# Optimization experiments

Hardware: AMD Instinct MI355X
Metric: run time of the kernel (lower is better)

## Reference

```python
import jax, jax.numpy as jnp
import numpy as np

H = 8
D = 512  # dmodel; each naive head projects to full D (not D//H)


def setup_inputs() -> dict:
    key = jax.random.key(0)
    ks = jax.random.split(key, 9)
    s = 1.0 / np.sqrt(D)
    x = jax.random.normal(ks[0], (2, 2048, D), dtype=jnp.float32)
    Wq = jax.random.normal(ks[1], (H, D, D), dtype=jnp.float32) * s
    Wk = jax.random.normal(ks[2], (H, D, D), dtype=jnp.float32) * s
    Wv = jax.random.normal(ks[3], (H, D, D), dtype=jnp.float32) * s
    bq = jnp.zeros((H, D), dtype=jnp.float32)
    bk = jnp.zeros((H, D), dtype=jnp.float32)
    bv = jnp.zeros((H, D), dtype=jnp.float32)
    Wo = jax.random.normal(ks[4], (H * D, D), dtype=jnp.float32) * (1.0 / np.sqrt(H * D))
    bo = jnp.zeros((D,), dtype=jnp.float32)
    return {"x": x, "Wq": Wq, "Wk": Wk, "Wv": Wv, "bq": bq, "bk": bk, "bv": bv, "Wo": Wo, "bo": bo}


def reference(x, Wq, Wk, Wv, bq, bk, bv, Wo, bo):
    # Batched form of the per-head Python loop: q/k/v -> [b, h, s, d]
    q = jnp.einsum("bsd,hde->bhse", x, Wq) + bq[None, :, None, :]
    k = jnp.einsum("bsd,hde->bhse", x, Wk) + bk[None, :, None, :]
    v = jnp.einsum("bsd,hde->bhse", x, Wv) + bv[None, :, None, :]
    scale = 1.0 / jnp.sqrt(jnp.asarray(D, dtype=x.dtype))
    scores = jnp.einsum("bhqe,bhke->bhqk", q, k) * scale  # [b, h, s, s]
    attn = jax.nn.softmax(scores, axis=-1)
    heads = jnp.einsum("bhqk,bhke->bhqe", attn, v)  # [b, h, s, d]
    b, h, s, d = heads.shape
    concat = jnp.transpose(heads, (0, 2, 1, 3)).reshape(b, s, h * d)  # concat on last axis
    out = concat @ Wo + bo  # output projection
    return out + x  # residual add
```

## Files before the change

### kernel.cpp

```cpp
#include <hip/hip_runtime.h>

typedef unsigned short u16;
typedef __attribute__((ext_vector_type(8))) short bh8;
typedef __attribute__((ext_vector_type(4))) float f32x4;
typedef __attribute__((ext_vector_type(4))) u16 us4;
typedef __attribute__((ext_vector_type(8))) u16 us8;

__device__ __forceinline__ u16 f2bf(float f){
  unsigned u = __builtin_bit_cast(unsigned, f);
  u += 0x7fffu + ((u >> 16) & 1u);
  return (u16)(u >> 16);
}
__device__ __forceinline__ float bf2f(u16 b){
  unsigned u = ((unsigned)b) << 16;
  return __builtin_bit_cast(float, u);
}

__device__ __forceinline__ void gload16(const void* g, void* l){
  __builtin_amdgcn_global_load_lds((const __attribute__((address_space(1))) unsigned*)g,
                                   (__attribute__((address_space(3))) unsigned*)l, 16, 0, 0);
}

template<int OUT_MODE>
__device__ __forceinline__ void gemm_core(
    u16* As, u16* Bs,
    const u16* __restrict__ A, int lda,
    const u16* __restrict__ B, int ldb,
    int K, float scale,
    const float* __restrict__ bias,
    float* __restrict__ lsum,
    const float* __restrict__ lraw,
    u16* __restrict__ outB, int ldo,
    int m0, int n0)
{
  const int t  = threadIdx.x;
  const int ln = t & 63;
  const int wv = t >> 6;
  const int wr = wv >> 1;
  const int wc = wv & 1;

  const int rs = t >> 2;
  const int cs = (t & 3) * 8;
  const u16* Ag0 = A + (size_t)(m0 + rs) * lda + cs;
  const u16* Ag1 = Ag0 + (size_t)64 * lda;
  const u16* Bg0 = B + (size_t)(n0 + rs) * ldb + cs;
  const u16* Bg1 = Bg0 + (size_t)64 * ldb;
  char* lA0 = (char*)As + wv * 1024;
  char* lA1 = lA0 + 4096;
  char* lB0 = (char*)Bs + wv * 1024;
  char* lB1 = lB0 + 4096;

  f32x4 acc[4][4] = {};

  const int frow = (ln & 15);
  const int fk   = (ln >> 4) * 8;

  for (int k0 = 0; k0 < K; k0 += 32){
    gload16(Ag0 + k0, lA0);
    gload16(Ag1 + k0, lA1);
    gload16(Bg0 + k0, lB0);
    gload16(Bg1 + k0, lB1);
    __syncthreads();
    bh8 a[4], b[4];
#pragma unroll
    for (int i = 0; i < 4; i++)
      a[i] = *(const bh8*)&As[(wr*64 + i*16 + frow)*32 + fk];
#pragma unroll
    for (int j = 0; j < 4; j++)
      b[j] = *(const bh8*)&Bs[(wc*64 + j*16 + frow)*32 + fk];
#pragma unroll
    for (int i = 0; i < 4; i++)
#pragma unroll
      for (int j = 0; j < 4; j++)
        acc[i][j] = __builtin_amdgcn_mfma_f32_16x16x32_bf16(a[i], b[j], acc[i][j], 0, 0, 0);
    __syncthreads();
  }

  const int col0 = ln & 15;
  const int r0   = (ln >> 4) * 4;
  float rsum[4][4];
#pragma unroll
  for (int i = 0; i < 4; i++){
    const int rowb = m0 + wr*64 + i*16 + r0;
#pragma unroll
    for (int q = 0; q < 4; q++) rsum[i][q] = 0.f;
#pragma unroll
    for (int j = 0; j < 4; j++){
      const int col = n0 + wc*64 + j*16 + col0;
      f32x4 v = acc[i][j];
      if (OUT_MODE == 1){
        const float bb = bias ? bias[col] : 0.f;
#pragma unroll
        for (int q = 0; q < 4; q++)
          outB[(size_t)(rowb + q) * ldo + col] = f2bf(v[q] * scale + bb);
      } else if (OUT_MODE == 2){
        const float bb = bias ? bias[col] : 0.f;
        us4 pk;
#pragma unroll
        for (int q = 0; q < 4; q++) pk[q] = f2bf(v[q] * scale + bb);
        *(us4*)&outB[(size_t)col * ldo + rowb] = pk;
      } else if (OUT_MODE == 3){
#pragma unroll
        for (int q = 0; q < 4; q++){
          float e = __expf(v[q] * scale);
          rsum[i][q] += e;
          outB[(size_t)(rowb + q) * ldo + col] = f2bf(e);
        }
      } else {
#pragma unroll
        for (int q = 0; q < 4; q++){
          float il = 1.0f / lraw[rowb + q];
          outB[(size_t)(rowb + q) * ldo + col] = f2bf(v[q] * il);
        }
      }
    }
    if (OUT_MODE == 3){
#pragma unroll
      for (int q = 0; q < 4; q++){
        float s = rsum[i][q];
        s += __shfl_xor(s, 1);
        s += __shfl_xor(s, 2);
        s += __shfl_xor(s, 4);
        s += __shfl_xor(s, 8);
        if ((ln & 15) == 0) atomicAdd(&lsum[rowb + q], s);
      }
    }
  }
}


__global__ __launch_bounds__(256) void k_qkv_qk(
    const u16* __restrict__ xb, const u16* __restrict__ WT,
    const float* __restrict__ bq, const float* __restrict__ bk,
    u16* __restrict__ Q, u16* __restrict__ Kb)
{
  __shared__ u16 As[4096], Bs[4096];
  const int z = blockIdx.z;
  const int p = z >> 4, bh = z & 15, b = bh >> 3, h = bh & 7;
  const u16* A = xb + (size_t)b * 2048 * 512;
  const u16* B = WT + (size_t)(p * 8 + h) * 512 * 512;
  const float* bias = (p == 0 ? bq : bk) + h * 512;
  u16* out = (p == 0 ? Q : Kb) + (size_t)bh * 2048 * 512;
  gemm_core<1>(As, Bs, A, 512, B, 512, 512, 1.f, bias, nullptr, nullptr,
               out, 512, blockIdx.y * 128, blockIdx.x * 128);
}

__global__ __launch_bounds__(256) void k_qkv_v(
    const u16* __restrict__ xb, const u16* __restrict__ WT,
    const float* __restrict__ bv, u16* __restrict__ VT)
{
  __shared__ u16 As[4096], Bs[4096];
  const int bh = blockIdx.z, b = bh >> 3, h = bh & 7;
  const u16* A = xb + (size_t)b * 2048 * 512;
  const u16* B = WT + (size_t)(16 + h) * 512 * 512;
  gemm_core<2>(As, Bs, A, 512, B, 512, 512, 1.f, bv + h * 512, nullptr, nullptr,
               VT + (size_t)bh * 512 * 2048, 2048,
               blockIdx.y * 128, blockIdx.x * 128);
}

__global__ __launch_bounds__(256) void k_score(
    const u16* __restrict__ Q, const u16* __restrict__ Kb,
    u16* __restrict__ scoresB, float* __restrict__ l, int bh0)
{
  __shared__ u16 As[4096], Bs[4096];
  const int z = blockIdx.z, bh = bh0 + z;
  gemm_core<3>(As, Bs, Q + (size_t)bh * 2048 * 512, 512,
               Kb + (size_t)bh * 2048 * 512, 512, 512,
               0.044194173824159216f , nullptr,
               l + (size_t)bh * 2048, nullptr,
               scoresB + (size_t)z * 2048 * 2048, 2048,
               blockIdx.y * 128, blockIdx.x * 128);
}

__global__ __launch_bounds__(256) void k_pv(
    const u16* __restrict__ scoresB, const u16* __restrict__ VT,
    const float* __restrict__ l, u16* __restrict__ concat, int bh0)
{
  __shared__ u16 As[4096], Bs[4096];
  const int z = blockIdx.z, bh = bh0 + z, b = bh >> 3, h = bh & 7;
  gemm_core<4>(As, Bs, scoresB + (size_t)z * 2048 * 2048, 2048,
               VT + (size_t)bh * 512 * 2048, 2048, 2048, 1.f, nullptr,
               nullptr, l + (size_t)bh * 2048,
               concat + (size_t)b * 2048 * 4096 + h * 512, 4096,
               blockIdx.y * 128, blockIdx.x * 128);
}

__global__ __launch_bounds__(256) void k_final_sk(
    const u16* __restrict__ concat, const u16* __restrict__ WoT,
    u16* __restrict__ partialB)
{
  __shared__ u16 As[4096], Bs[4096];
  const int sk = blockIdx.z;
  gemm_core<1>(As, Bs, concat + sk * 1024, 4096,
               WoT + sk * 1024, 4096, 1024, 1.f, nullptr, nullptr, nullptr,
               partialB + (size_t)sk * 4096 * 512, 512,
               blockIdx.y * 128, blockIdx.x * 128);
}

__global__ __launch_bounds__(256) void k_reduce(
    const u16* __restrict__ partialB, const float* __restrict__ bo,
    const float* __restrict__ x, float* __restrict__ out)
{
  const size_t i4 = ((size_t)blockIdx.x * 256 + threadIdx.x) * 4;
  const int col = (int)(i4 & 511);
  float4 s = *(const float4*)(x + i4);
  s.x += bo[col]; s.y += bo[col + 1]; s.z += bo[col + 2]; s.w += bo[col + 3];
#pragma unroll
  for (int sk = 0; sk < 4; sk++){
    us4 p = *(const us4*)(partialB + (size_t)sk * 2097152 + i4);
    s.x += bf2f(p[0]); s.y += bf2f(p[1]); s.z += bf2f(p[2]); s.w += bf2f(p[3]);
  }
  *(float4*)(out + i4) = s;
}


__global__ void k_convx(const float* __restrict__ x, u16* __restrict__ xb)
{
  const int i = blockIdx.x * blockDim.x + threadIdx.x;
  float4 v = *(const float4*)(x + (size_t)i * 4);
  us4 o; o[0] = f2bf(v.x); o[1] = f2bf(v.y); o[2] = f2bf(v.z); o[3] = f2bf(v.w);
  *(us4*)(xb + (size_t)i * 4) = o;
}

__global__ void k_transpose_qkv(const float* __restrict__ Wq,
                                const float* __restrict__ Wk,
                                const float* __restrict__ Wv,
                                u16* __restrict__ WT)
{
  __shared__ float tile[32][33];
  const int z = blockIdx.z, p = z >> 3, h = z & 7;
  const float* ip = (p == 0 ? Wq : p == 1 ? Wk : Wv) + (size_t)h * 512 * 512;
  u16* op = WT + (size_t)z * 512 * 512;
  const int c0 = blockIdx.x * 32, r0 = blockIdx.y * 32;
  const int tx = threadIdx.x, ty = threadIdx.y;
#pragma unroll
  for (int m = 0; m < 4; m++)
    tile[ty + m * 8][tx] = ip[(size_t)(r0 + ty + m * 8) * 512 + c0 + tx];
  __syncthreads();
#pragma unroll
  for (int m = 0; m < 4; m++)
    op[(size_t)(c0 + ty + m * 8) * 512 + r0 + tx] = f2bf(tile[tx][ty + m * 8]);
}

__global__ void k_transpose_f2b(const float* __restrict__ in, u16* __restrict__ out,
                                int rows, int cols)
{
  __shared__ float tile[32][33];
  const int c0 = blockIdx.x * 32, r0 = blockIdx.y * 32;
  const int tx = threadIdx.x, ty = threadIdx.y;
#pragma unroll
  for (int m = 0; m < 4; m++)
    tile[ty + m * 8][tx] = in[(size_t)(r0 + ty + m * 8) * cols + c0 + tx];
  __syncthreads();
#pragma unroll
  for (int m = 0; m < 4; m++)
    out[(size_t)(c0 + ty + m * 8) * rows + r0 + tx] = f2bf(tile[tx][ty + m * 8]);
}


extern "C" void kernel_launch(void* const* d_in, const int* in_sizes, int n_in,
                              void* d_out, int out_size, void* d_ws, size_t ws_size,
                              hipStream_t stream)
{
  const float* x  = (const float*)d_in[0];
  const float* Wq = (const float*)d_in[1];
  const float* Wk = (const float*)d_in[2];
  const float* Wv = (const float*)d_in[3];
  const float* bq = (const float*)d_in[4];
  const float* bk = (const float*)d_in[5];
  const float* bv = (const float*)d_in[6];
  const float* Wo = (const float*)d_in[7];
  const float* bo = (const float*)d_in[8];
  float* out = (float*)d_out;

  char* w = (char*)d_ws;
  size_t off = 0;
  auto alloc = [&](size_t bytes) -> char* {
    char* p = w + off; off += (bytes + 255) & ~(size_t)255; return p;
  };
  u16* xb   = (u16*)alloc(4096ull * 512 * 2);
  u16* WT   = (u16*)alloc(3ull * 8 * 512 * 512 * 2);
  u16* WoT  = (u16*)alloc(512ull * 4096 * 2);
  u16* Q    = (u16*)alloc(16ull * 2048 * 512 * 2);
  u16* Kb   = (u16*)alloc(16ull * 2048 * 512 * 2);
  u16* VT   = (u16*)alloc(16ull * 512 * 2048 * 2);
  u16* conc = (u16*)alloc(4096ull * 4096 * 2);
  u16* part = (u16*)alloc(4ull * 4096 * 512 * 2);
  float* l  = (float*)alloc(16ull * 2048 * 4);
  const size_t scoreBytes = 2048ull * 2048 * 2;
  int CH = 16;
  while (CH > 1 && off + (size_t)CH * scoreBytes > ws_size) CH >>= 1;
  u16* scores = (u16*)alloc((size_t)CH * scoreBytes);

  hipMemsetAsync(l, 0, 16ull * 2048 * 4, stream);

  k_convx<<<2048, 256, 0, stream>>>(x, xb);
  dim3 tb(32, 8);
  k_transpose_qkv<<<dim3(16, 16, 24), tb, 0, stream>>>(Wq, Wk, Wv, WT);
  k_transpose_f2b<<<dim3(16, 128, 1), tb, 0, stream>>>(Wo, WoT, 4096, 512);

  k_qkv_qk<<<dim3(4, 16, 32), 256, 0, stream>>>(xb, WT, bq, bk, Q, Kb);
  k_qkv_v <<<dim3(4, 16, 16), 256, 0, stream>>>(xb, WT, bv, VT);

  for (int c = 0; c < 16; c += CH){
    k_score<<<dim3(16, 16, CH), 256, 0, stream>>>(Q, Kb, scores, l, c);
    k_pv   <<<dim3(4, 16, CH), 256, 0, stream>>>(scores, VT, l, conc, c);
  }

  k_final_sk<<<dim3(4, 32, 4), 256, 0, stream>>>(conc, WoT, part);
  k_reduce<<<2048, 256, 0, stream>>>(part, bo, x, out);
}
```

Before: 465.6 us.

## Merge prep kernels, fuse QKV launches, and atomically reduce the output projection

```diff
diff --git a/kernel.cpp b/kernel.cpp
--- a/kernel.cpp
+++ b/kernel.cpp
@@ -4,24 +4,19 @@
 typedef __attribute__((ext_vector_type(8))) short bh8;
 typedef __attribute__((ext_vector_type(4))) float f32x4;
 typedef __attribute__((ext_vector_type(4))) u16 us4;
-typedef __attribute__((ext_vector_type(8))) u16 us8;
 
 __device__ __forceinline__ u16 f2bf(float f){
   unsigned u = __builtin_bit_cast(unsigned, f);
   u += 0x7fffu + ((u >> 16) & 1u);
   return (u16)(u >> 16);
 }
-__device__ __forceinline__ float bf2f(u16 b){
-  unsigned u = ((unsigned)b) << 16;
-  return __builtin_bit_cast(float, u);
-}
 
 __device__ __forceinline__ void gload16(const void* g, void* l){
   __builtin_amdgcn_global_load_lds((const __attribute__((address_space(1))) unsigned*)g,
                                    (__attribute__((address_space(3))) unsigned*)l, 16, 0, 0);
 }
 
-template<int OUT_MODE>
+template<int MODE>
 __device__ __forceinline__ void gemm_core(
     u16* As, u16* Bs,
     const u16* __restrict__ A, int lda,
@@ -30,7 +25,7 @@
     const float* __restrict__ bias,
     float* __restrict__ lsum,
     const float* __restrict__ lraw,
-    u16* __restrict__ outB, int ldo,
+    u16* __restrict__ outB, float* __restrict__ outF, int ldo,
     int m0, int n0)
 {
   const int t  = threadIdx.x;
@@ -78,46 +73,49 @@
 
   const int col0 = ln & 15;
   const int r0   = (ln >> 4) * 4;
-  float rsum[4][4];
 #pragma unroll
   for (int i = 0; i < 4; i++){
     const int rowb = m0 + wr*64 + i*16 + r0;
-#pragma unroll
-    for (int q = 0; q < 4; q++) rsum[i][q] = 0.f;
+    float rsum[4] = {0.f, 0.f, 0.f, 0.f};
+    float il[4];
+    if (MODE == 4){
+#pragma unroll
+      for (int q = 0; q < 4; q++) il[q] = 1.0f / lraw[rowb + q];
+    }
 #pragma unroll
     for (int j = 0; j < 4; j++){
       const int col = n0 + wc*64 + j*16 + col0;
       f32x4 v = acc[i][j];
-      if (OUT_MODE == 1){
+      if (MODE == 1){
         const float bb = bias ? bias[col] : 0.f;
 #pragma unroll
         for (int q = 0; q < 4; q++)
           outB[(size_t)(rowb + q) * ldo + col] = f2bf(v[q] * scale + bb);
-      } else if (OUT_MODE == 2){
-        const float bb = bias ? bias[col] : 0.f;
-        us4 pk;
-#pragma unroll
-        for (int q = 0; q < 4; q++) pk[q] = f2bf(v[q] * scale + bb);
-        *(us4*)&outB[(size_t)col * ldo + rowb] = pk;
-      } else if (OUT_MODE == 3){
+      } else if (MODE == 3){
 #pragma unroll
         for (int q = 0; q < 4; q++){
           float e = __expf(v[q] * scale);
-          rsum[i][q] += e;
+          rsum[q] += e;
           outB[(size_t)(rowb + q) * ldo + col] = f2bf(e);
         }
+      } else if (MODE == 4){
+#pragma unroll
+        for (int q = 0; q < 4; q++)
+          outB[(size_t)(rowb + q) * ldo + col] = f2bf(v[q] * il[q]);
+      } else if (MODE == 5){
+#pragma unroll
+        for (int q = 0; q < 4; q++)
+          outB[(size_t)(rowb + q) * ldo + col] = f2bf(v[q] * scale + bias[rowb + q]);
       } else {
 #pragma unroll
-        for (int q = 0; q < 4; q++){
-          float il = 1.0f / lraw[rowb + q];
-          outB[(size_t)(rowb + q) * ldo + col] = f2bf(v[q] * il);
-        }
+        for (int q = 0; q < 4; q++)
+          atomicAdd(&outF[(size_t)(rowb + q) * ldo + col], v[q]);
       }
     }
-    if (OUT_MODE == 3){
+    if (MODE == 3){
 #pragma unroll
       for (int q = 0; q < 4; q++){
-        float s = rsum[i][q];
+        float s = rsum[q];
         s += __shfl_xor(s, 1);
         s += __shfl_xor(s, 2);
         s += __shfl_xor(s, 4);
@@ -128,34 +126,97 @@
   }
 }
 
-
-__global__ __launch_bounds__(256) void k_qkv_qk(
+__global__ __launch_bounds__(256) void k_prep(
+    const float* __restrict__ x,
+    const float* __restrict__ Wq, const float* __restrict__ Wk,
+    const float* __restrict__ Wv, const float* __restrict__ Wo,
+    const float* __restrict__ bo,
+    u16* __restrict__ xb, u16* __restrict__ WT, u16* __restrict__ WoT,
+    float* __restrict__ l, float* __restrict__ out)
+{
+  __shared__ float tile[32][33];
+  int bid = blockIdx.x;
+  const int t = threadIdx.x;
+  if (bid < 2048){
+    const size_t i4 = ((size_t)bid * 256 + t) * 4;
+    float4 v = *(const float4*)(x + i4);
+    us4 o; o[0] = f2bf(v.x); o[1] = f2bf(v.y); o[2] = f2bf(v.z); o[3] = f2bf(v.w);
+    *(us4*)(xb + i4) = o;
+    return;
+  }
+  bid -= 2048;
+  if (bid < 6144){
+    const int z = bid >> 8, tid = bid & 255;
+    const int bx = tid & 15, by = tid >> 4;
+    const int p = z >> 3, h = z & 7;
+    const float* ip = (p == 0 ? Wq : p == 1 ? Wk : Wv) + (size_t)h * 512 * 512;
+    u16* op = WT + (size_t)z * 512 * 512;
+    const int tx = t & 31, ty = t >> 5;
+    const int c0 = bx * 32, r0 = by * 32;
+#pragma unroll
+    for (int m = 0; m < 4; m++)
+      tile[ty + m * 8][tx] = ip[(size_t)(r0 + ty + m * 8) * 512 + c0 + tx];
+    __syncthreads();
+#pragma unroll
+    for (int m = 0; m < 4; m++)
+      op[(size_t)(c0 + ty + m * 8) * 512 + r0 + tx] = f2bf(tile[tx][ty + m * 8]);
+    return;
+  }
+  bid -= 6144;
+  if (bid < 2048){
+    const int bx = bid & 15, by = bid >> 4;
+    const int tx = t & 31, ty = t >> 5;
+    const int c0 = bx * 32, r0 = by * 32;
+#pragma unroll
+    for (int m = 0; m < 4; m++)
+      tile[ty + m * 8][tx] = Wo[(size_t)(r0 + ty + m * 8) * 512 + c0 + tx];
+    __syncthreads();
+#pragma unroll
+    for (int m = 0; m < 4; m++)
+      WoT[(size_t)(c0 + ty + m * 8) * 4096 + r0 + tx] = f2bf(tile[tx][ty + m * 8]);
+    return;
+  }
+  bid -= 2048;
+  if (bid < 2048){
+    const size_t i4 = ((size_t)bid * 256 + t) * 4;
+    const int col = (int)(i4 & 511);
+    float4 v = *(const float4*)(x + i4);
+    v.x += bo[col]; v.y += bo[col + 1]; v.z += bo[col + 2]; v.w += bo[col + 3];
+    *(float4*)(out + i4) = v;
+    return;
+  }
+  bid -= 2048;
+  {
+    const int i = bid * 256 + t;
+    if (i < 32768) l[i] = 0.f;
+  }
+}
+
+__global__ __launch_bounds__(256) void k_qkv(
     const u16* __restrict__ xb, const u16* __restrict__ WT,
     const float* __restrict__ bq, const float* __restrict__ bk,
-    u16* __restrict__ Q, u16* __restrict__ Kb)
+    const float* __restrict__ bv,
+    u16* __restrict__ Q, u16* __restrict__ Kb, u16* __restrict__ VT)
 {
   __shared__ u16 As[4096], Bs[4096];
   const int z = blockIdx.z;
   const int p = z >> 4, bh = z & 15, b = bh >> 3, h = bh & 7;
-  const u16* A = xb + (size_t)b * 2048 * 512;
-  const u16* B = WT + (size_t)(p * 8 + h) * 512 * 512;
-  const float* bias = (p == 0 ? bq : bk) + h * 512;
-  u16* out = (p == 0 ? Q : Kb) + (size_t)bh * 2048 * 512;
-  gemm_core<1>(As, Bs, A, 512, B, 512, 512, 1.f, bias, nullptr, nullptr,
-               out, 512, blockIdx.y * 128, blockIdx.x * 128);
-}
-
-__global__ __launch_bounds__(256) void k_qkv_v(
-    const u16* __restrict__ xb, const u16* __restrict__ WT,
-    const float* __restrict__ bv, u16* __restrict__ VT)
-{
-  __shared__ u16 As[4096], Bs[4096];
-  const int bh = blockIdx.z, b = bh >> 3, h = bh & 7;
-  const u16* A = xb + (size_t)b * 2048 * 512;
-  const u16* B = WT + (size_t)(16 + h) * 512 * 512;
-  gemm_core<2>(As, Bs, A, 512, B, 512, 512, 1.f, bv + h * 512, nullptr, nullptr,
-               VT + (size_t)bh * 512 * 2048, 2048,
-               blockIdx.y * 128, blockIdx.x * 128);
+  if (p < 2){
+    const u16* A = xb + (size_t)b * 2048 * 512;
+    const u16* B = WT + (size_t)(p * 8 + h) * 512 * 512;
+    const float* bias = (p == 0 ? bq : bk) + h * 512;
+    u16* o = (p == 0 ? Q : Kb) + (size_t)bh * 2048 * 512;
+    gemm_core<1>(As, Bs, A, 512, B, 512, 512, 1.f, bias, nullptr, nullptr,
+                 o, nullptr, 512, blockIdx.y * 128, blockIdx.x * 128);
+  } else {
+    const int tid = blockIdx.y * 4 + blockIdx.x;
+    const int m0 = (tid >> 4) * 128;
+    const int n0 = (tid & 15) * 128;
+    gemm_core<5>(As, Bs, WT + (size_t)(16 + h) * 512 * 512, 512,
+                 xb + (size_t)b * 2048 * 512, 512, 512, 1.f, bv + h * 512,
+                 nullptr, nullptr, VT + (size_t)bh * 512 * 2048, nullptr, 2048,
+                 m0, n0);
+  }
 }
 
 __global__ __launch_bounds__(256) void k_score(
@@ -168,7 +229,7 @@
                Kb + (size_t)bh * 2048 * 512, 512, 512,
                0.044194173824159216f , nullptr,
                l + (size_t)bh * 2048, nullptr,
-               scoresB + (size_t)z * 2048 * 2048, 2048,
+               scoresB + (size_t)z * 2048 * 2048, nullptr, 2048,
                blockIdx.y * 128, blockIdx.x * 128);
 }
 
@@ -181,80 +242,19 @@
   gemm_core<4>(As, Bs, scoresB + (size_t)z * 2048 * 2048, 2048,
                VT + (size_t)bh * 512 * 2048, 2048, 2048, 1.f, nullptr,
                nullptr, l + (size_t)bh * 2048,
-               concat + (size_t)b * 2048 * 4096 + h * 512, 4096,
+               concat + (size_t)b * 2048 * 4096 + h * 512, nullptr, 4096,
                blockIdx.y * 128, blockIdx.x * 128);
 }
 
-__global__ __launch_bounds__(256) void k_final_sk(
+__global__ __launch_bounds__(256) void k_final(
     const u16* __restrict__ concat, const u16* __restrict__ WoT,
-    u16* __restrict__ partialB)
+    float* __restrict__ out)
 {
   __shared__ u16 As[4096], Bs[4096];
   const int sk = blockIdx.z;
-  gemm_core<1>(As, Bs, concat + sk * 1024, 4096,
+  gemm_core<6>(As, Bs, concat + sk * 1024, 4096,
                WoT + sk * 1024, 4096, 1024, 1.f, nullptr, nullptr, nullptr,
-               partialB + (size_t)sk * 4096 * 512, 512,
-               blockIdx.y * 128, blockIdx.x * 128);
-}
-
-__global__ __launch_bounds__(256) void k_reduce(
-    const u16* __restrict__ partialB, const float* __restrict__ bo,
-    const float* __restrict__ x, float* __restrict__ out)
-{
-  const size_t i4 = ((size_t)blockIdx.x * 256 + threadIdx.x) * 4;
-  const int col = (int)(i4 & 511);
-  float4 s = *(const float4*)(x + i4);
-  s.x += bo[col]; s.y += bo[col + 1]; s.z += bo[col + 2]; s.w += bo[col + 3];
-#pragma unroll
-  for (int sk = 0; sk < 4; sk++){
-    us4 p = *(const us4*)(partialB + (size_t)sk * 2097152 + i4);
-    s.x += bf2f(p[0]); s.y += bf2f(p[1]); s.z += bf2f(p[2]); s.w += bf2f(p[3]);
-  }
-  *(float4*)(out + i4) = s;
-}
-
-
-__global__ void k_convx(const float* __restrict__ x, u16* __restrict__ xb)
-{
-  const int i = blockIdx.x * blockDim.x + threadIdx.x;
-  float4 v = *(const float4*)(x + (size_t)i * 4);
-  us4 o; o[0] = f2bf(v.x); o[1] = f2bf(v.y); o[2] = f2bf(v.z); o[3] = f2bf(v.w);
-  *(us4*)(xb + (size_t)i * 4) = o;
-}
-
-__global__ void k_transpose_qkv(const float* __restrict__ Wq,
-                                const float* __restrict__ Wk,
-                                const float* __restrict__ Wv,
-                                u16* __restrict__ WT)
-{
-  __shared__ float tile[32][33];
-  const int z = blockIdx.z, p = z >> 3, h = z & 7;
-  const float* ip = (p == 0 ? Wq : p == 1 ? Wk : Wv) + (size_t)h * 512 * 512;
-  u16* op = WT + (size_t)z * 512 * 512;
-  const int c0 = blockIdx.x * 32, r0 = blockIdx.y * 32;
-  const int tx = threadIdx.x, ty = threadIdx.y;
-#pragma unroll
-  for (int m = 0; m < 4; m++)
-    tile[ty + m * 8][tx] = ip[(size_t)(r0 + ty + m * 8) * 512 + c0 + tx];
-  __syncthreads();
-#pragma unroll
-  for (int m = 0; m < 4; m++)
-    op[(size_t)(c0 + ty + m * 8) * 512 + r0 + tx] = f2bf(tile[tx][ty + m * 8]);
-}
-
-__global__ void k_transpose_f2b(const float* __restrict__ in, u16* __restrict__ out,
-                                int rows, int cols)
-{
-  __shared__ float tile[32][33];
-  const int c0 = blockIdx.x * 32, r0 = blockIdx.y * 32;
-  const int tx = threadIdx.x, ty = threadIdx.y;
-#pragma unroll
-  for (int m = 0; m < 4; m++)
-    tile[ty + m * 8][tx] = in[(size_t)(r0 + ty + m * 8) * cols + c0 + tx];
-  __syncthreads();
-#pragma unroll
-  for (int m = 0; m < 4; m++)
-    out[(size_t)(c0 + ty + m * 8) * rows + r0 + tx] = f2bf(tile[tx][ty + m * 8]);
+               nullptr, out, 512, blockIdx.y * 128, blockIdx.x * 128);
 }
 
 
@@ -285,28 +285,20 @@
   u16* Kb   = (u16*)alloc(16ull * 2048 * 512 * 2);
   u16* VT   = (u16*)alloc(16ull * 512 * 2048 * 2);
   u16* conc = (u16*)alloc(4096ull * 4096 * 2);
-  u16* part = (u16*)alloc(4ull * 4096 * 512 * 2);
   float* l  = (float*)alloc(16ull * 2048 * 4);
   const size_t scoreBytes = 2048ull * 2048 * 2;
   int CH = 16;
   while (CH > 1 && off + (size_t)CH * scoreBytes > ws_size) CH >>= 1;
   u16* scores = (u16*)alloc((size_t)CH * scoreBytes);
 
-  hipMemsetAsync(l, 0, 16ull * 2048 * 4, stream);
-
-  k_convx<<<2048, 256, 0, stream>>>(x, xb);
-  dim3 tb(32, 8);
-  k_transpose_qkv<<<dim3(16, 16, 24), tb, 0, stream>>>(Wq, Wk, Wv, WT);
-  k_transpose_f2b<<<dim3(16, 128, 1), tb, 0, stream>>>(Wo, WoT, 4096, 512);
-
-  k_qkv_qk<<<dim3(4, 16, 32), 256, 0, stream>>>(xb, WT, bq, bk, Q, Kb);
-  k_qkv_v <<<dim3(4, 16, 16), 256, 0, stream>>>(xb, WT, bv, VT);
+  k_prep<<<12416, 256, 0, stream>>>(x, Wq, Wk, Wv, Wo, bo, xb, WT, WoT, l, out);
+
+  k_qkv<<<dim3(4, 16, 48), 256, 0, stream>>>(xb, WT, bq, bk, bv, Q, Kb, VT);
 
   for (int c = 0; c < 16; c += CH){
     k_score<<<dim3(16, 16, CH), 256, 0, stream>>>(Q, Kb, scores, l, c);
     k_pv   <<<dim3(4, 16, CH), 256, 0, stream>>>(scores, VT, l, conc, c);
   }
 
-  k_final_sk<<<dim3(4, 32, 4), 256, 0, stream>>>(conc, WoT, part);
-  k_reduce<<<2048, 256, 0, stream>>>(part, bo, x, out);
-}
+  k_final<<<dim3(4, 32, 4), 256, 0, stream>>>(conc, WoT, out);
+}
```

New measurement: 463.8 us. No clear change (-0.4%).
